# Kernel tuning notes

Measured on AMD Instinct MI355X. Metric: run time of the kernel, lower is better.

## Reference

```python
import jax, jax.numpy as jnp
import numpy as np
from jax import lax

EPS = 1e-12
ALPHA = 20.0
TEMP = 10.0
TAU = 0.45
LAMBDA_N = 0.3
REP_W = 0.15
MOMENTUM = 0.9
N_SINK_ITER = 3


def _norm(x):
    # F.normalize(p=2, dim=1, eps=1e-12)
    return x / jnp.maximum(jnp.linalg.norm(x, axis=-1, keepdims=True), EPS)


def sinkhorn(sim, alpha=ALPHA, n_iterations=N_SINK_ITER):
    Q = jnp.exp(alpha * sim).T  # [K, B]
    K, B = Q.shape
    Q = Q / jnp.sum(Q)
    for _ in range(n_iterations):
        Q = Q / (jnp.sum(Q, axis=1, keepdims=True) * K)
        Q = Q / (jnp.sum(Q, axis=0, keepdims=True) * B)
    return (Q * B).T  # [B, K]


def update_negative_centers(n_feats, positive_center, negative_centers):
    # all under no_grad in the original
    nf = _norm(n_feats)
    pos = _norm(positive_center)
    sim_to_pos = (nf @ pos.T)[:, 0]                       # [Nn]
    keep = sim_to_pos < 0.7
    negc = _norm(negative_centers)
    sim = nf @ negc.T                                     # [Nn, K]
    assign = jnp.argmax(sim, axis=1)
    K = negative_centers.shape[0]
    onehot = jax.nn.one_hot(assign, K, dtype=n_feats.dtype) * keep[:, None].astype(n_feats.dtype)
    counts = jnp.sum(onehot, axis=0)                      # [K]
    sums = onehot.T @ n_feats                             # [K, D] masked per-cluster sums of raw feats
    means = sums / jnp.maximum(counts[:, None], 1.0)
    new_center = _norm(means)
    lerped = negative_centers + (new_center - negative_centers) * (1.0 - MOMENTUM)
    lerped = lerped / jnp.maximum(jnp.linalg.norm(lerped, axis=1, keepdims=True), EPS)
    # update only clusters with >=3 assigned kept features (skips everything if keep.sum()==0)
    return jnp.where((counts >= 3.0)[:, None], lerped, negative_centers)


def setup_inputs() -> dict:
    key = jax.random.key(0)
    ks = jax.random.split(key, 6)
    dim, n_proxies, n_centers = 512, 1024, 4
    return {
        'p_feats': jax.random.normal(ks[0], (16384, dim), jnp.float32),
        'u_feats': jax.random.normal(ks[1], (65536, dim), jnp.float32),
        'n_feats': jax.random.normal(ks[2], (32768, dim), jnp.float32),
        'positive_center': _norm(jax.random.normal(ks[3], (1, dim), jnp.float32)),
        'proxy_u': jax.random.normal(ks[4], (n_proxies, dim), jnp.float32),
        'negative_centers': _norm(jax.random.normal(ks[5], (n_centers, dim), jnp.float32)),
    }


def reference(p_feats, u_feats, n_feats, positive_center, proxy_u, negative_centers):
    pos = lax.stop_gradient(positive_center)   # requires_grad=False param
    negc0 = lax.stop_gradient(negative_centers)  # buffer

    # l_loss: mean(1 - cos(pos, p_feats))
    dist = _norm(pos) @ _norm(p_feats).T       # [1, Np]
    l_loss = jnp.mean(1.0 - dist)

    # EMA update of negative centers (no_grad)
    negc = lax.stop_gradient(update_negative_centers(lax.stop_gradient(n_feats), pos, negc0))

    # n branch: self-distillation on negative centers
    sim_n = _norm(n_feats) @ _norm(negc).T     # [Nn, K]
    target_n = jax.nn.softmax(sim_n, axis=1)
    loss_n = -jnp.mean(jnp.sum(target_n * jax.nn.log_softmax(sim_n, axis=1), axis=1))

    # pseudo-label branch on u_feats vs negative centers (sinkhorn targets, detached)
    sim_u_neg = _norm(u_feats) @ _norm(negc).T  # [Nu, K]
    soft_assign = sinkhorn(lax.stop_gradient(sim_u_neg))
    loss_pseudo = -jnp.mean(jnp.sum(soft_assign * jax.nn.log_softmax(sim_u_neg, axis=1), axis=1))

    n_loss = (loss_n + loss_pseudo) / 2.0

    # u branch vs learnable proxies
    u_similarity = _norm(u_feats) @ _norm(proxy_u).T  # [Nu, P]
    u_target = sinkhorn(lax.stop_gradient(u_similarity))
    u_loss = -jnp.mean(jnp.sum(u_target * jax.nn.log_softmax(u_similarity * TEMP, axis=1), axis=1))

    # repulsion
    sim_np = (_norm(negc) @ _norm(pos).T)[:, 0]       # [K]
    rep_np = -jnp.mean(jnp.log(jnp.clip(1.0 - sim_np, 1e-6, None)))
    nc = _norm(negc)
    sim_nn = nc @ nc.T                                 # [K, K]
    K = negc.shape[0]
    offdiag = ~jnp.eye(K, dtype=bool)
    logs = jnp.where(offdiag, jnp.log(jnp.clip(1.0 - sim_nn, 1e-6, None)), 0.0)
    rep_nn = -jnp.sum(logs) / (K * K - K)
    repulsion_loss = rep_np + 0.1 * rep_nn

    cls_loss = TAU * l_loss + LAMBDA_N * n_loss + (0.55 - TAU) * u_loss + REP_W * repulsion_loss
    return cls_loss, l_loss, u_loss, n_loss, repulsion_loss
```

## Files before the change

kernel.cpp:

```cpp
#include <hip/hip_runtime.h>
#include <hip/hip_bf16.h>

typedef __attribute__((ext_vector_type(8))) short short8;
typedef __attribute__((ext_vector_type(8))) unsigned short ushort8;
typedef __attribute__((ext_vector_type(4))) float f32x4;

#define EPSN 1e-12f
#define GN 1024
#define GK 512

__device__ __forceinline__ float bf2f(unsigned short h) {
  union { unsigned int u; float f; } c; c.u = ((unsigned int)h) << 16; return c.f;
}
__device__ __forceinline__ unsigned short f2bf(float f) {
  union { float f; unsigned int u; } c; c.f = f;
  unsigned int u = c.u;
  return (unsigned short)((u + 0x7fffu + ((u >> 16) & 1u)) >> 16);
}
__device__ __forceinline__ float wredsum(float v) {
  v += __shfl_xor(v, 32); v += __shfl_xor(v, 16); v += __shfl_xor(v, 8);
  v += __shfl_xor(v, 4);  v += __shfl_xor(v, 2);  v += __shfl_xor(v, 1);
  return v;
}

#define GLL(g, l) __builtin_amdgcn_global_load_lds( \
    (const __attribute__((address_space(1))) unsigned int*)(g), \
    (__attribute__((address_space(3))) unsigned int*)(l), 16, 0, 0)

__global__ void k_prep(const float* __restrict__ pc, const float* __restrict__ nc,
                       float* __restrict__ pos_hat, float* __restrict__ negc0_hat) {
  int tid = threadIdx.x, lane = tid & 63, w = tid >> 6;
  const float* src = (w == 0) ? pc : (nc + (w - 1) * 512);
  float* dst = (w == 0) ? pos_hat : (negc0_hat + (w - 1) * 512);
  float4 a = *(const float4*)(src + lane * 8);
  float4 b = *(const float4*)(src + lane * 8 + 4);
  float x[8] = {a.x,a.y,a.z,a.w,b.x,b.y,b.z,b.w};
  float ss = 0.f;
  #pragma unroll
  for (int j = 0; j < 8; j++) ss += x[j]*x[j];
  ss = wredsum(ss);
  float inv = 1.f / fmaxf(sqrtf(ss), EPSN);
  #pragma unroll
  for (int j = 0; j < 8; j++) dst[lane*8+j] = x[j]*inv;
}

__global__ __launch_bounds__(256) void k_redcol(const float* __restrict__ P, float* __restrict__ R,
                                                int nrows, int ncols) {
  __shared__ float lred[64];
  int tid = threadIdx.x, lane = tid & 63, w = tid >> 6;
  int colg = blockIdx.x * 16;
  int ci = tid & 15;
  int r0 = tid >> 4;
  float s = 0.f;
  for (int r = r0; r < nrows; r += 16)
    s += P[(size_t)r * ncols + colg + ci];
  s += __shfl_xor(s, 16); s += __shfl_xor(s, 32);
  if (lane < 16) lred[w * 16 + lane] = s;
  __syncthreads();
  if (tid < 16) R[colg + tid] = lred[tid] + lred[16 + tid] + lred[32 + tid] + lred[48 + tid];
}

__global__ __launch_bounds__(256) void k_rownormP(const float* __restrict__ X,
                                                  unsigned short* __restrict__ Y,
                                                  float* __restrict__ invn, int rows) {
  int lane = threadIdx.x & 63;
  int w0 = blockIdx.x * 4 + (threadIdx.x >> 6);
  int nw = gridDim.x * 4;
  for (int row = w0; row < rows; row += nw) {
    const float* src = X + (size_t)row * 512 + lane * 8;
    float4 a = *(const float4*)src;
    float4 b = *(const float4*)(src + 4);
    float x[8] = {a.x,a.y,a.z,a.w,b.x,b.y,b.z,b.w};
    float ss = 0.f;
    #pragma unroll
    for (int j = 0; j < 8; j++) ss += x[j]*x[j];
    ss = wredsum(ss);
    float inv = 1.f / fmaxf(sqrtf(ss), EPSN);
    if (lane == 0) invn[row] = inv;
    ushort8 o;
    #pragma unroll
    for (int j = 0; j < 8; j++) o[j] = f2bf(x[j]);
    *(ushort8*)(Y + (size_t)row * 512 + lane * 8) = o;
  }
}

__global__ __launch_bounds__(256) void k_ploss(const float* __restrict__ PF, const float* __restrict__ ph_g,
                                               float* __restrict__ PlossP) {
  __shared__ float lred[4];
  int tid = threadIdx.x, lane = tid & 63, w = tid >> 6;
  float ph[8];
  #pragma unroll
  for (int j = 0; j < 8; j++) ph[j] = ph_g[lane*8+j];
  float lsum = 0.f;
  int row0 = blockIdx.x * 32;
  for (int rr = w; rr < 32; rr += 4) {
    int row = row0 + rr;
    const float* src = PF + (size_t)row * 512 + lane * 8;
    float4 a = *(const float4*)src;
    float4 b = *(const float4*)(src + 4);
    float x[8] = {a.x,a.y,a.z,a.w,b.x,b.y,b.z,b.w};
    float ss = 0.f, dp = 0.f;
    #pragma unroll
    for (int j = 0; j < 8; j++) { ss += x[j]*x[j]; dp += x[j]*ph[j]; }
    ss = wredsum(ss); dp = wredsum(dp);
    if (lane == 0) lsum += dp / fmaxf(sqrtf(ss), EPSN);
  }
  if (lane == 0) lred[w] = lsum;
  __syncthreads();
  if (tid == 0) PlossP[blockIdx.x] = lred[0]+lred[1]+lred[2]+lred[3];
}

__global__ __launch_bounds__(256) void k_nstats(const float* __restrict__ NF, const float* __restrict__ ph_g,
                                                const float* __restrict__ nch0, float* __restrict__ inv_n,
                                                float* __restrict__ CntP, float* __restrict__ SumP) {
  __shared__ float fl[8192];
  __shared__ float cb[16];
  int tid = threadIdx.x, lane = tid & 63, w = tid >> 6;
  float ph[8], nh[4][8];
  #pragma unroll
  for (int j = 0; j < 8; j++) ph[j] = ph_g[lane*8+j];
  #pragma unroll
  for (int c = 0; c < 4; c++)
    #pragma unroll
    for (int j = 0; j < 8; j++) nh[c][j] = nch0[c*512 + lane*8 + j];
  float acc[4][8];
  float cnt[4] = {0.f,0.f,0.f,0.f};
  #pragma unroll
  for (int c = 0; c < 4; c++)
    #pragma unroll
    for (int j = 0; j < 8; j++) acc[c][j] = 0.f;
  int row0 = blockIdx.x * 64;
  for (int rr = w; rr < 64; rr += 4) {
    int row = row0 + rr;
    const float* src = NF + (size_t)row * 512 + lane * 8;
    float4 a = *(const float4*)src;
    float4 b = *(const float4*)(src + 4);
    float x[8] = {a.x,a.y,a.z,a.w,b.x,b.y,b.z,b.w};
    float ss = 0.f, dp = 0.f, dn[4] = {0.f,0.f,0.f,0.f};
    #pragma unroll
    for (int j = 0; j < 8; j++) {
      ss += x[j]*x[j]; dp += x[j]*ph[j];
      #pragma unroll
      for (int c = 0; c < 4; c++) dn[c] += x[j]*nh[c][j];
    }
    ss = wredsum(ss); dp = wredsum(dp);
    #pragma unroll
    for (int c = 0; c < 4; c++) dn[c] = wredsum(dn[c]);
    float inv = 1.f / fmaxf(sqrtf(ss), EPSN);
    if (lane == 0) inv_n[row] = inv;
    float sp = dp * inv;
    float s0 = dn[0]*inv, s1 = dn[1]*inv, s2 = dn[2]*inv, s3 = dn[3]*inv;
    int am = 0; float best = s0;
    if (s1 > best) { best = s1; am = 1; }
    if (s2 > best) { best = s2; am = 2; }
    if (s3 > best) { best = s3; am = 3; }
    float kf = (sp < 0.7f) ? 1.f : 0.f;
    #pragma unroll
    for (int c = 0; c < 4; c++) {
      float m = (am == c) ? kf : 0.f;
      #pragma unroll
      for (int j = 0; j < 8; j++) acc[c][j] += m * x[j];
      if (lane == 0) cnt[c] += m;
    }
  }
  #pragma unroll
  for (int c = 0; c < 4; c++)
    #pragma unroll
    for (int j = 0; j < 8; j++) fl[w*2048 + c*512 + lane*8 + j] = acc[c][j];
  if (lane == 0) {
    #pragma unroll
    for (int c = 0; c < 4; c++) cb[w*4+c] = cnt[c];
  }
  __syncthreads();
  for (int q = tid; q < 2048; q += 256)
    SumP[(size_t)blockIdx.x * 2048 + q] = fl[q] + fl[2048+q] + fl[4096+q] + fl[6144+q];
  if (tid < 4) CntP[blockIdx.x * 4 + tid] = cb[tid] + cb[4+tid] + cb[8+tid] + cb[12+tid];
}

__global__ void k_center(const float* __restrict__ CntP, const float* __restrict__ sums,
                         const float* __restrict__ negc_raw, const float* __restrict__ pos_hat,
                         float* __restrict__ negc_hat, float* __restrict__ scal) {
  __shared__ float hbuf[2048];
  __shared__ float spn[4];
  __shared__ float snn[16];
  int tid = threadIdx.x, lane = tid & 63, c = tid >> 6;
  float cs = 0.f;
  for (int r = lane; r < 512; r += 64) cs += CntP[r*4 + c];
  float cnt = wredsum(cs);
  float x[8], raw[8], ph[8];
  #pragma unroll
  for (int j = 0; j < 8; j++) {
    x[j] = sums[c*512 + lane*8 + j] / fmaxf(cnt, 1.f);
    raw[j] = negc_raw[c*512 + lane*8 + j];
    ph[j] = pos_hat[lane*8 + j];
  }
  float ss = 0.f;
  #pragma unroll
  for (int j = 0; j < 8; j++) ss += x[j]*x[j];
  ss = wredsum(ss);
  float n1 = fmaxf(sqrtf(ss), EPSN);
  #pragma unroll
  for (int j = 0; j < 8; j++) x[j] = raw[j] + (x[j]/n1 - raw[j]) * 0.1f;
  ss = 0.f;
  #pragma unroll
  for (int j = 0; j < 8; j++) ss += x[j]*x[j];
  ss = wredsum(ss);
  float n2 = fmaxf(sqrtf(ss), EPSN);
  bool upd = (cnt >= 3.0f);
  #pragma unroll
  for (int j = 0; j < 8; j++) x[j] = upd ? (x[j]/n2) : raw[j];
  ss = 0.f;
  #pragma unroll
  for (int j = 0; j < 8; j++) ss += x[j]*x[j];
  ss = wredsum(ss);
  float n3 = fmaxf(sqrtf(ss), EPSN);
  float dp = 0.f;
  #pragma unroll
  for (int j = 0; j < 8; j++) {
    x[j] = x[j] / n3;
    negc_hat[c*512 + lane*8 + j] = x[j];
    hbuf[c*512 + lane*8 + j] = x[j];
    dp += x[j] * ph[j];
  }
  dp = wredsum(dp);
  if (lane == 0) spn[c] = dp;
  __syncthreads();
  float d4[4] = {0.f,0.f,0.f,0.f};
  #pragma unroll
  for (int c2 = 0; c2 < 4; c2++) {
    float d = 0.f;
    #pragma unroll
    for (int j = 0; j < 8; j++) d += x[j] * hbuf[c2*512 + lane*8 + j];
    d4[c2] = wredsum(d);
  }
  if (lane == 0) {
    #pragma unroll
    for (int c2 = 0; c2 < 4; c2++) snn[c*4 + c2] = d4[c2];
  }
  __syncthreads();
  if (tid == 0) {
    float rep_np = 0.f;
    for (int i = 0; i < 4; i++) rep_np += logf(fmaxf(1.f - spn[i], 1e-6f));
    rep_np = -rep_np * 0.25f;
    float rep_nn = 0.f;
    for (int i = 0; i < 4; i++)
      for (int j2 = 0; j2 < 4; j2++)
        if (i != j2) rep_nn += logf(fmaxf(1.f - snn[i*4+j2], 1e-6f));
    rep_nn = -rep_nn / 12.f;
    scal[4] = rep_np + 0.1f * rep_nn;
  }
}

__global__ __launch_bounds__(256) void k_nloss(const float* __restrict__ NF, const float* __restrict__ inv_n,
                                               const float* __restrict__ nch, float* __restrict__ NlossP) {
  __shared__ float lred[4];
  int tid = threadIdx.x, lane = tid & 63, w = tid >> 6;
  float nh[4][8];
  #pragma unroll
  for (int c = 0; c < 4; c++)
    #pragma unroll
    for (int j = 0; j < 8; j++) nh[c][j] = nch[c*512 + lane*8 + j];
  float lsum = 0.f;
  int row0 = blockIdx.x * 32;
  for (int rr = w; rr < 32; rr += 4) {
    int row = row0 + rr;
    const float* src = NF + (size_t)row * 512 + lane * 8;
    float4 a = *(const float4*)src;
    float4 b = *(const float4*)(src + 4);
    float x[8] = {a.x,a.y,a.z,a.w,b.x,b.y,b.z,b.w};
    float dn[4] = {0.f,0.f,0.f,0.f};
    #pragma unroll
    for (int j = 0; j < 8; j++)
      #pragma unroll
      for (int c = 0; c < 4; c++) dn[c] += x[j]*nh[c][j];
    #pragma unroll
    for (int c = 0; c < 4; c++) dn[c] = wredsum(dn[c]);
    if (lane == 0) {
      float inv = inv_n[row];
      float s0 = dn[0]*inv, s1 = dn[1]*inv, s2 = dn[2]*inv, s3 = dn[3]*inv;
      float mx = fmaxf(fmaxf(s0,s1), fmaxf(s2,s3));
      float e0 = __expf(s0-mx), e1 = __expf(s1-mx), e2 = __expf(s2-mx), e3 = __expf(s3-mx);
      float Z = e0+e1+e2+e3;
      lsum += (mx + logf(Z)) - (e0*s0+e1*s1+e2*s2+e3*s3)/Z;
    }
  }
  if (lane == 0) lred[w] = lsum;
  __syncthreads();
  if (tid == 0) NlossP[blockIdx.x] = lred[0]+lred[1]+lred[2]+lred[3];
}

__global__ __launch_bounds__(256) void k_upass(const float* __restrict__ U, const float* __restrict__ nch,
                                               float* __restrict__ SU, float* __restrict__ UPp,
                                               unsigned short* __restrict__ Uh, float* __restrict__ invU) {
  __shared__ float ub[16];
  int tid = threadIdx.x, lane = tid & 63, w = tid >> 6;
  float nh[4][8];
  #pragma unroll
  for (int c = 0; c < 4; c++)
    #pragma unroll
    for (int j = 0; j < 8; j++) nh[c][j] = nch[c*512 + lane*8 + j];
  float eacc[4] = {0.f,0.f,0.f,0.f};
  int row0 = blockIdx.x * 32;
  for (int rr = w; rr < 32; rr += 4) {
    int row = row0 + rr;
    const float* src = U + (size_t)row * 512 + lane * 8;
    float4 a = *(const float4*)src;
    float4 b = *(const float4*)(src + 4);
    float x[8] = {a.x,a.y,a.z,a.w,b.x,b.y,b.z,b.w};
    float ss = 0.f, dn[4] = {0.f,0.f,0.f,0.f};
    #pragma unroll
    for (int j = 0; j < 8; j++) {
      ss += x[j]*x[j];
      #pragma unroll
      for (int c = 0; c < 4; c++) dn[c] += x[j]*nh[c][j];
    }
    ss = wredsum(ss);
    #pragma unroll
    for (int c = 0; c < 4; c++) dn[c] = wredsum(dn[c]);
    float inv = 1.f / fmaxf(sqrtf(ss), EPSN);
    ushort8 o;
    #pragma unroll
    for (int j = 0; j < 8; j++) o[j] = f2bf(x[j]);
    *(ushort8*)(Uh + (size_t)row * 512 + lane * 8) = o;
    if (lane == 0) {
      invU[row] = inv;
      float4 sv; sv.x = dn[0]*inv; sv.y = dn[1]*inv; sv.z = dn[2]*inv; sv.w = dn[3]*inv;
      *(float4*)(SU + (size_t)row * 4) = sv;
      eacc[0] += __expf(20.f*sv.x); eacc[1] += __expf(20.f*sv.y);
      eacc[2] += __expf(20.f*sv.z); eacc[3] += __expf(20.f*sv.w);
    }
  }
  if (lane == 0) {
    #pragma unroll
    for (int c = 0; c < 4; c++) ub[w*4+c] = eacc[c];
  }
  __syncthreads();
  if (tid < 4) UPp[blockIdx.x * 4 + tid] = ub[tid] + ub[4+tid] + ub[8+tid] + ub[12+tid];
}

__global__ __launch_bounds__(256) void k_psink(const float* __restrict__ SU, const float* __restrict__ Pin,
                                               int n_in, float* __restrict__ Pout,
                                               float* __restrict__ PLout, int mode) {
  __shared__ float lr[16];
  int tid = threadIdx.x, lane = tid & 63, w = tid >> 6;
  float i0 = 0.f, i1 = 0.f, i2 = 0.f, i3 = 0.f;
  for (int r = tid; r < n_in; r += 256) {
    float4 v = *(const float4*)(Pin + (size_t)r * 4);
    i0 += v.x; i1 += v.y; i2 += v.z; i3 += v.w;
  }
  i0 = wredsum(i0); i1 = wredsum(i1); i2 = wredsum(i2); i3 = wredsum(i3);
  if (lane == 0) { lr[w*4+0] = i0; lr[w*4+1] = i1; lr[w*4+2] = i2; lr[w*4+3] = i3; }
  __syncthreads();
  float R0 = lr[0]+lr[4]+lr[8]+lr[12];
  float R1_ = lr[1]+lr[5]+lr[9]+lr[13];
  float R2_ = lr[2]+lr[6]+lr[10]+lr[14];
  float R3_ = lr[3]+lr[7]+lr[11]+lr[15];
  float r0 = 1.f/(4.f*R0), r1 = 1.f/(4.f*R1_), r2 = 1.f/(4.f*R2_), r3 = 1.f/(4.f*R3_);
  float a0 = 0.f, a1 = 0.f, a2 = 0.f, a3 = 0.f, lsum = 0.f;
  int row = blockIdx.x * blockDim.x + threadIdx.x;
  {
    float4 s = *(const float4*)(SU + (size_t)row * 4);
    float x0 = __expf(20.f*s.x), x1 = __expf(20.f*s.y);
    float x2 = __expf(20.f*s.z), x3 = __expf(20.f*s.w);
    float E0 = x0*r0, E1 = x1*r1, E2 = x2*r2, E3 = x3*r3;
    float cf = 1.f / ((E0+E1+E2+E3) * 65536.f);
    if (mode == 1) { a0 = x0*cf; a1 = x1*cf; a2 = x2*cf; a3 = x3*cf; }
    else {
      float term = (E0*s.x + E1*s.y + E2*s.z + E3*s.w) * 65536.f * cf;
      float mx = fmaxf(fmaxf(s.x,s.y), fmaxf(s.z,s.w));
      float z = __expf(s.x-mx)+__expf(s.y-mx)+__expf(s.z-mx)+__expf(s.w-mx);
      lsum = (mx + logf(z)) - term;
    }
  }
  __syncthreads();
  if (mode == 1) {
    a0 = wredsum(a0); a1 = wredsum(a1); a2 = wredsum(a2); a3 = wredsum(a3);
    if (lane == 0) { lr[w*4+0] = a0; lr[w*4+1] = a1; lr[w*4+2] = a2; lr[w*4+3] = a3; }
    __syncthreads();
    if (tid < 4) Pout[blockIdx.x * 4 + tid] = lr[tid] + lr[4+tid] + lr[8+tid] + lr[12+tid];
  } else {
    lsum = wredsum(lsum);
    if (lane == 0) lr[w] = lsum;
    __syncthreads();
    if (tid == 0) PLout[blockIdx.x] = lr[0]+lr[1]+lr[2]+lr[3];
  }
}

__global__ __launch_bounds__(512) void k_gemm(const unsigned short* __restrict__ A,
                                              const unsigned short* __restrict__ B,
                                              const float* __restrict__ invU,
                                              const float* __restrict__ invP,
                                              unsigned short* __restrict__ S,
                                              float* __restrict__ R1) {
  __shared__ unsigned short lAB[24576];
  __shared__ float red[1024];
  unsigned short* lA = lAB;
  unsigned short* lB = lAB + 16384;
  const int swz = (blockIdx.x & 7) * 256 + (blockIdx.x >> 3);
  const int rowblk = swz >> 3, colblk = swz & 7;
  const int tid = threadIdx.x, lane = tid & 63;
  const int wid = tid >> 6, wm = wid >> 1, wn = wid & 1;
  f32x4 acc[4][4];
  #pragma unroll
  for (int m = 0; m < 4; m++)
    #pragma unroll
    for (int n = 0; n < 4; n++) acc[m][n] = (f32x4){0.f,0.f,0.f,0.f};
  const unsigned short* Ag = A + (size_t)rowblk * 256 * GK;
  const unsigned short* Bg = B + (size_t)colblk * 128 * GK;
  const int r0 = tid >> 3;
  const int c0 = ((tid & 7) ^ (r0 & 7)) * 8;
  for (int kt = 0; kt < GK; kt += 64) {
    #pragma unroll
    for (int i = 0; i < 4; i++)
      GLL(Ag + (size_t)(r0 + i*64) * GK + kt + c0, lA + (i*512 + tid) * 8);
    #pragma unroll
    for (int i = 0; i < 2; i++)
      GLL(Bg + (size_t)(r0 + i*64) * GK + kt + c0, lB + (i*512 + tid) * 8);
    __syncthreads();
    #pragma unroll
    for (int kk = 0; kk < 2; kk++) {
      short8 af[4], bf[4];
      #pragma unroll
      for (int m = 0; m < 4; m++) {
        int rowA = wm*64 + m*16 + (lane & 15);
        int ch = ((kk*4 + (lane >> 4)) ^ (rowA & 7)) * 8;
        af[m] = *(const short8*)(lA + rowA * 64 + ch);
      }
      #pragma unroll
      for (int n = 0; n < 4; n++) {
        int rowB = wn*64 + n*16 + (lane & 15);
        int ch = ((kk*4 + (lane >> 4)) ^ (rowB & 7)) * 8;
        bf[n] = *(const short8*)(lB + rowB * 64 + ch);
      }
      #pragma unroll
      for (int m = 0; m < 4; m++)
        #pragma unroll
        for (int n = 0; n < 4; n++)
          acc[m][n] = __builtin_amdgcn_mfma_f32_16x16x32_bf16(af[m], bf[n], acc[m][n], 0, 0, 0);
    }
    __syncthreads();
  }
  unsigned short* lC = lAB;
  float racc[16];
  #pragma unroll
  for (int j = 0; j < 16; j++) racc[j] = 0.f;
  const size_t outbase = (size_t)rowblk * 256 * GN + (size_t)colblk * 128;
  const int ch8 = lane & 7, rsub = lane >> 3;
  #pragma unroll
  for (int h = 0; h < 2; h++) {
    if ((wm >> 1) == h) {
      #pragma unroll
      for (int m = 0; m < 4; m++)
        #pragma unroll
        for (int n = 0; n < 4; n++) {
          int col = wn*64 + n*16 + (lane & 15);
          float ip = invP[colblk * 128 + col];
          #pragma unroll
          for (int r = 0; r < 4; r++) {
            int lr2 = (wm & 1)*64 + m*16 + ((lane >> 4) << 2) + r;
            float iu = invU[rowblk * 256 + h*128 + lr2];
            lC[lr2 * 136 + col] = f2bf(acc[m][n][r] * iu * ip);
          }
        }
    }
    __syncthreads();
    #pragma unroll
    for (int it = 0; it < 2; it++) {
      int lr2 = it*64 + wid*8 + rsub;
      int grow = h*128 + lr2;
      ushort8 v0 = *(const ushort8*)(lC + lr2 * 136 + ch8 * 8);
      ushort8 v1 = *(const ushort8*)(lC + lr2 * 136 + 64 + ch8 * 8);
      *(short8*)(S + outbase + (size_t)grow * GN + ch8 * 8) = (short8)v0;
      *(short8*)(S + outbase + (size_t)grow * GN + 64 + ch8 * 8) = (short8)v1;
      #pragma unroll
      for (int j = 0; j < 8; j++) {
        racc[j]     += __expf(20.f * bf2f(v0[j]));
        racc[8 + j] += __expf(20.f * bf2f(v1[j]));
      }
    }
    __syncthreads();
  }
  #pragma unroll
  for (int j = 0; j < 16; j++) {
    racc[j] += __shfl_xor(racc[j], 8);
    racc[j] += __shfl_xor(racc[j], 16);
    racc[j] += __shfl_xor(racc[j], 32);
  }
  if (lane < 8) {
    #pragma unroll
    for (int j = 0; j < 8; j++) {
      red[wid * 128 + lane * 8 + j]      = racc[j];
      red[wid * 128 + 64 + lane * 8 + j] = racc[8 + j];
    }
  }
  __syncthreads();
  if (tid < 128) {
    float s8 = 0.f;
    #pragma unroll
    for (int i = 0; i < 8; i++) s8 += red[i * 128 + tid];
    int gcol = colblk * 128 + tid;
    int q = (gcol & 15) * 64 + (gcol >> 4);
    atomicAdd(&R1[q], s8);
  }
}

__global__ __launch_bounds__(256) void k_sink1(const unsigned short* __restrict__ S,
                                               const float* __restrict__ Rin,
                                               float* __restrict__ Pout) {
  __shared__ float lds[4096];
  int tid = threadIdx.x, lane = tid & 63, w = tid >> 6;
  float rj[16];
  #pragma unroll
  for (int j = 0; j < 16; j++) rj[j] = 1.f / (1024.f * Rin[j*64 + lane]);
  float acc[16];
  #pragma unroll
  for (int j = 0; j < 16; j++) acc[j] = 0.f;
  int row0 = blockIdx.x * 32;
  for (int rr = w; rr < 16; rr += 4) {
    const unsigned short* SrA = S + (size_t)(row0 + rr) * 1024 + lane * 16;
    const unsigned short* SrB = S + (size_t)(row0 + rr + 16) * 1024 + lane * 16;
    ushort8 a0 = *(const ushort8*)SrA, a1 = *(const ushort8*)(SrA + 8);
    ushort8 b0 = *(const ushort8*)SrB, b1 = *(const ushort8*)(SrB + 8);
    float XA[16], XB[16];
    float csA = 0.f, csB = 0.f;
    #pragma unroll
    for (int j = 0; j < 8; j++) {
      XA[j]   = __expf(20.f * bf2f(a0[j]));
      XA[8+j] = __expf(20.f * bf2f(a1[j]));
      XB[j]   = __expf(20.f * bf2f(b0[j]));
      XB[8+j] = __expf(20.f * bf2f(b1[j]));
    }
    #pragma unroll
    for (int j = 0; j < 16; j++) { csA += XA[j]*rj[j]; csB += XB[j]*rj[j]; }
    #pragma unroll
    for (int d = 32; d >= 1; d >>= 1) {
      csA += __shfl_xor(csA, d);
      csB += __shfl_xor(csB, d);
    }
    float cfA = 1.f / (csA * 65536.f), cfB = 1.f / (csB * 65536.f);
    #pragma unroll
    for (int j = 0; j < 16; j++) acc[j] += XA[j]*cfA + XB[j]*cfB;
  }
  #pragma unroll
  for (int j = 0; j < 16; j++) lds[w*1024 + lane + 64*j] = acc[j];
  __syncthreads();
  for (int q = tid; q < 1024; q += 256)
    Pout[(size_t)blockIdx.x * 1024 + q] = lds[q] + lds[1024+q] + lds[2048+q] + lds[3072+q];
}

__global__ __launch_bounds__(256) void k_sinkL(const unsigned short* __restrict__ S,
                                               const float* __restrict__ Rin,
                                               float* __restrict__ LPout) {
  __shared__ float lr[4];
  int tid = threadIdx.x, lane = tid & 63, w = tid >> 6;
  float rj[16];
  #pragma unroll
  for (int j = 0; j < 16; j++) rj[j] = 1.f / (1024.f * Rin[j*64 + lane]);
  float lsum = 0.f;
  int row0 = blockIdx.x * 32;
  for (int rr = w; rr < 16; rr += 4) {
    const unsigned short* SrA = S + (size_t)(row0 + rr) * 1024 + lane * 16;
    const unsigned short* SrB = S + (size_t)(row0 + rr + 16) * 1024 + lane * 16;
    ushort8 a0 = *(const ushort8*)SrA, a1 = *(const ushort8*)(SrA + 8);
    ushort8 b0 = *(const ushort8*)SrB, b1 = *(const ushort8*)(SrB + 8);
    float sA[16], sB[16], yA[16], yB[16];
    #pragma unroll
    for (int j = 0; j < 8; j++) {
      sA[j] = bf2f(a0[j]); sA[8+j] = bf2f(a1[j]);
      sB[j] = bf2f(b0[j]); sB[8+j] = bf2f(b1[j]);
    }
    #pragma unroll
    for (int j = 0; j < 16; j++) { yA[j] = __expf(10.f*sA[j]); yB[j] = __expf(10.f*sB[j]); }
    float csA = 0.f, csB = 0.f, tA = 0.f, tB = 0.f, YA = 0.f, YB = 0.f;
    #pragma unroll
    for (int j = 0; j < 16; j++) {
      float xa = yA[j]*yA[j]*rj[j];
      float xb = yB[j]*yB[j]*rj[j];
      csA += xa; tA += xa*sA[j]; YA += yA[j];
      csB += xb; tB += xb*sB[j]; YB += yB[j];
    }
    #pragma unroll
    for (int d = 32; d >= 1; d >>= 1) {
      csA += __shfl_xor(csA, d); csB += __shfl_xor(csB, d);
      tA  += __shfl_xor(tA, d);  tB  += __shfl_xor(tB, d);
      YA  += __shfl_xor(YA, d);  YB  += __shfl_xor(YB, d);
    }
    if (lane == 0)
      lsum += (logf(YA) - 10.f*tA/csA) + (logf(YB) - 10.f*tB/csB);
  }
  if (lane == 0) lr[w] = lsum;
  __syncthreads();
  if (tid == 0) LPout[blockIdx.x] = lr[0]+lr[1]+lr[2]+lr[3];
}

__global__ __launch_bounds__(256) void k_final(const float* __restrict__ scal,
                                               const float* __restrict__ PlossP,
                                               const float* __restrict__ NlossP,
                                               const float* __restrict__ PLp,
                                               const float* __restrict__ SLp,
                                               float* __restrict__ out) {
  __shared__ float lr[4];
  int tid = threadIdx.x, lane = tid & 63, w = tid >> 6;
  float tots[4];
  const float* arrs[4] = {PlossP, NlossP, PLp, SLp};
  const int ns[4] = {512, 1024, 256, 2048};
  for (int k = 0; k < 4; k++) {
    float s = 0.f;
    for (int i = tid; i < ns[k]; i += 256) s += arrs[k][i];
    s = wredsum(s);
    __syncthreads();
    if (lane == 0) lr[w] = s;
    __syncthreads();
    tots[k] = lr[0]+lr[1]+lr[2]+lr[3];
  }
  if (tid == 0) {
    float l   = 1.f - tots[0] / 16384.f;
    float ln  = tots[1] / 32768.f;
    float lp  = tots[2] / 65536.f;
    float ul  = tots[3] / 65536.f;
    float rep = scal[4];
    float nl  = 0.5f * (ln + lp);
    float cls = 0.45f*l + 0.3f*nl + 0.1f*ul + 0.15f*rep;
    out[0] = cls;
    out[1] = l;
    out[2] = ul;
    out[3] = nl;
    out[4] = rep;
  }
}

extern "C" void kernel_launch(void* const* d_in, const int* in_sizes, int n_in,
                              void* d_out, int out_size, void* d_ws, size_t ws_size,
                              hipStream_t stream) {
  const float* PF = (const float*)d_in[0];
  const float* UF = (const float*)d_in[1];
  const float* NF = (const float*)d_in[2];
  const float* PC = (const float*)d_in[3];
  const float* PU = (const float*)d_in[4];
  const float* NC = (const float*)d_in[5];

  char* ws = (char*)d_ws;
  const size_t WS_REQUIRED = 202736768ULL;
  if (ws_size < WS_REQUIRED) return;

  float* R1     = (float*)(ws + 0);
  float* R2     = (float*)(ws + 4096);
  float* R3     = (float*)(ws + 8192);
  float* scal   = (float*)(ws + 12288);
  float* sums   = (float*)(ws + 12416);
  float* invP   = (float*)(ws + 20608);
  float* UPp    = (float*)(ws + 24704);
  float* PPpA   = (float*)(ws + 57472);
  float* PPpB   = (float*)(ws + 61568);
  float* PLp    = (float*)(ws + 65664);
  float* PlossP = (float*)(ws + 66688);
  float* NlossP = (float*)(ws + 68736);
  float* CntP   = (float*)(ws + 72832);
  float* pos_hat   = (float*)(ws + 81024);
  float* negc0_hat = (float*)(ws + 83072);
  float* negc_hat  = (float*)(ws + 91264);
  float* invU      = (float*)(ws + 99456);
  float* inv_n = (float*)(ws + 361600);
  float* SU    = (float*)(ws + 361600);
  unsigned short* Ph = (unsigned short*)(ws + 361600);
  float* SumP = (float*)(ws + 1410176);
  unsigned short* Uh = (unsigned short*)(ws + 1410176);
  float* SPp  = (float*)(ws + 1410176);
  float* SLp  = (float*)(ws + 9798784);
  unsigned short* S = (unsigned short*)(ws + 68519040);

  hipMemsetAsync(ws, 0, 4096, stream);

  k_prep<<<1, 320, 0, stream>>>(PC, NC, pos_hat, negc0_hat);
  k_ploss<<<512, 256, 0, stream>>>(PF, pos_hat, PlossP);
  k_nstats<<<512, 256, 0, stream>>>(NF, pos_hat, negc0_hat, inv_n, CntP, SumP);
  k_redcol<<<128, 256, 0, stream>>>(SumP, sums, 512, 2048);
  k_center<<<1, 256, 0, stream>>>(CntP, sums, NC, pos_hat, negc_hat, scal);
  k_nloss<<<1024, 256, 0, stream>>>(NF, inv_n, negc_hat, NlossP);
  k_upass<<<2048, 256, 0, stream>>>(UF, negc_hat, SU, UPp, Uh, invU);

  k_psink<<<256, 256, 0, stream>>>(SU, UPp, 2048, PPpA, nullptr, 1);
  k_psink<<<256, 256, 0, stream>>>(SU, PPpA, 256, PPpB, nullptr, 1);
  k_psink<<<256, 256, 0, stream>>>(SU, PPpB, 256, nullptr, PLp, 2);

  k_rownormP<<<32, 256, 0, stream>>>(PU, Ph, invP, 1024);

  k_gemm<<<2048, 512, 0, stream>>>(Uh, Ph, invU, invP, S, R1);
  k_sink1<<<2048, 256, 0, stream>>>(S, R1, SPp);
  k_redcol<<<64, 256, 0, stream>>>(SPp, R2, 2048, 1024);
  k_sink1<<<2048, 256, 0, stream>>>(S, R2, SPp);
  k_redcol<<<64, 256, 0, stream>>>(SPp, R3, 2048, 1024);
  k_sinkL<<<2048, 256, 0, stream>>>(S, R3, SLp);

  k_final<<<1, 256, 0, stream>>>(scal, PlossP, NlossP, PLp, SLp, (float*)d_out);
}
```

Measured before the change: 419.0 us.

## Double-buffer GEMM LDS tiles with k=32 steps and split nstats across more blocks

The bf16 GEMM main loop now uses two LDS buffers of 32-wide K tiles. The next tile's global-to-LDS load is issued before the MFMAs on the current tile, so memory latency overlaps compute and there is one barrier per step. The XOR swizzle is dropped, which may bring back LDS bank conflicts on the fragment reads. Separately, the negative-stats kernel now handles 32 rows per block over 1024 blocks for more parallelism, and its partial-count buffer moves to a larger workspace region, which doubles the partial-sum reduction work.

```diff
diff --git a/kernel.cpp b/kernel.cpp
--- a/kernel.cpp
+++ b/kernel.cpp
@@ -129,8 +129,8 @@
   for (int c = 0; c < 4; c++)
     #pragma unroll
     for (int j = 0; j < 8; j++) acc[c][j] = 0.f;
-  int row0 = blockIdx.x * 64;
-  for (int rr = w; rr < 64; rr += 4) {
+  int row0 = blockIdx.x * 32;
+  for (int rr = w; rr < 32; rr += 4) {
     int row = row0 + rr;
     const float* src = NF + (size_t)row * 512 + lane * 8;
     float4 a = *(const float4*)src;
@@ -185,7 +185,7 @@
   __shared__ float snn[16];
   int tid = threadIdx.x, lane = tid & 63, c = tid >> 6;
   float cs = 0.f;
-  for (int r = lane; r < 512; r += 64) cs += CntP[r*4 + c];
+  for (int r = lane; r < 1024; r += 64) cs += CntP[r*4 + c];
   float cnt = wredsum(cs);
   float x[8], raw[8], ph[8];
   #pragma unroll
@@ -394,8 +394,6 @@
                                               float* __restrict__ R1) {
   __shared__ unsigned short lAB[24576];
   __shared__ float red[1024];
-  unsigned short* lA = lAB;
-  unsigned short* lB = lAB + 16384;
   const int swz = (blockIdx.x & 7) * 256 + (blockIdx.x >> 3);
   const int rowblk = swz >> 3, colblk = swz & 7;
   const int tid = threadIdx.x, lane = tid & 63;
@@ -407,38 +405,37 @@
     for (int n = 0; n < 4; n++) acc[m][n] = (f32x4){0.f,0.f,0.f,0.f};
   const unsigned short* Ag = A + (size_t)rowblk * 256 * GK;
   const unsigned short* Bg = B + (size_t)colblk * 128 * GK;
-  const int r0 = tid >> 3;
-  const int c0 = ((tid & 7) ^ (r0 & 7)) * 8;
-  for (int kt = 0; kt < GK; kt += 64) {
-    #pragma unroll
-    for (int i = 0; i < 4; i++)
-      GLL(Ag + (size_t)(r0 + i*64) * GK + kt + c0, lA + (i*512 + tid) * 8);
-    #pragma unroll
-    for (int i = 0; i < 2; i++)
-      GLL(Bg + (size_t)(r0 + i*64) * GK + kt + c0, lB + (i*512 + tid) * 8);
+  const int sr = tid >> 2;
+  const int sc = (tid & 3) * 8;
+  GLL(Ag + (size_t)sr * GK + sc,         lAB + tid * 8);
+  GLL(Ag + (size_t)(sr + 128) * GK + sc, lAB + (512 + tid) * 8);
+  GLL(Bg + (size_t)sr * GK + sc,         lAB + 8192 + tid * 8);
+  __syncthreads();
+  int cur = 0;
+  for (int kt16 = 0; kt16 < 16; kt16++) {
+    if (kt16 < 15) {
+      unsigned short* nb = lAB + (cur ^ 1) * 12288;
+      const int kt = (kt16 + 1) * 32;
+      GLL(Ag + (size_t)sr * GK + kt + sc,         nb + tid * 8);
+      GLL(Ag + (size_t)(sr + 128) * GK + kt + sc, nb + (512 + tid) * 8);
+      GLL(Bg + (size_t)sr * GK + kt + sc,         nb + 8192 + tid * 8);
+    }
+    const unsigned short* cA = lAB + cur * 12288;
+    const unsigned short* cB = cA + 8192;
+    short8 af[4], bf[4];
+    #pragma unroll
+    for (int m = 0; m < 4; m++)
+      af[m] = *(const short8*)(cA + (wm*64 + m*16 + (lane & 15)) * 32 + (lane >> 4) * 8);
+    #pragma unroll
+    for (int n = 0; n < 4; n++)
+      bf[n] = *(const short8*)(cB + (wn*64 + n*16 + (lane & 15)) * 32 + (lane >> 4) * 8);
+    #pragma unroll
+    for (int m = 0; m < 4; m++)
+      #pragma unroll
+      for (int n = 0; n < 4; n++)
+        acc[m][n] = __builtin_amdgcn_mfma_f32_16x16x32_bf16(af[m], bf[n], acc[m][n], 0, 0, 0);
     __syncthreads();
-    #pragma unroll
-    for (int kk = 0; kk < 2; kk++) {
-      short8 af[4], bf[4];
-      #pragma unroll
-      for (int m = 0; m < 4; m++) {
-        int rowA = wm*64 + m*16 + (lane & 15);
-        int ch = ((kk*4 + (lane >> 4)) ^ (rowA & 7)) * 8;
-        af[m] = *(const short8*)(lA + rowA * 64 + ch);
-      }
-      #pragma unroll
-      for (int n = 0; n < 4; n++) {
-        int rowB = wn*64 + n*16 + (lane & 15);
-        int ch = ((kk*4 + (lane >> 4)) ^ (rowB & 7)) * 8;
-        bf[n] = *(const short8*)(lB + rowB * 64 + ch);
-      }
-      #pragma unroll
-      for (int m = 0; m < 4; m++)
-        #pragma unroll
-        for (int n = 0; n < 4; n++)
-          acc[m][n] = __builtin_amdgcn_mfma_f32_16x16x32_bf16(af[m], bf[n], acc[m][n], 0, 0, 0);
-    }
-    __syncthreads();
+    cur ^= 1;
   }
   unsigned short* lC = lAB;
   float racc[16];
@@ -655,7 +652,6 @@
   float* PLp    = (float*)(ws + 65664);
   float* PlossP = (float*)(ws + 66688);
   float* NlossP = (float*)(ws + 68736);
-  float* CntP   = (float*)(ws + 72832);
   float* pos_hat   = (float*)(ws + 81024);
   float* negc0_hat = (float*)(ws + 83072);
   float* negc_hat  = (float*)(ws + 91264);
@@ -667,14 +663,15 @@
   unsigned short* Uh = (unsigned short*)(ws + 1410176);
   float* SPp  = (float*)(ws + 1410176);
   float* SLp  = (float*)(ws + 9798784);
+  float* CntP = (float*)(ws + 9806976);
   unsigned short* S = (unsigned short*)(ws + 68519040);
 
   hipMemsetAsync(ws, 0, 4096, stream);
 
   k_prep<<<1, 320, 0, stream>>>(PC, NC, pos_hat, negc0_hat);
   k_ploss<<<512, 256, 0, stream>>>(PF, pos_hat, PlossP);
-  k_nstats<<<512, 256, 0, stream>>>(NF, pos_hat, negc0_hat, inv_n, CntP, SumP);
-  k_redcol<<<128, 256, 0, stream>>>(SumP, sums, 512, 2048);
+  k_nstats<<<1024, 256, 0, stream>>>(NF, pos_hat, negc0_hat, inv_n, CntP, SumP);
+  k_redcol<<<128, 256, 0, stream>>>(SumP, sums, 1024, 2048);
   k_center<<<1, 256, 0, stream>>>(CntP, sums, NC, pos_hat, negc_hat, scal);
   k_nloss<<<1024, 256, 0, stream>>>(NF, inv_n, negc_hat, NlossP);
   k_upass<<<2048, 256, 0, stream>>>(UF, negc_hat, SU, UPp, Uh, invU);
```

Result: slower. 464.7 us (+10.9%).
